# Kernel tuning notes

Hardware: AMD Instinct MI355X
Metric: run time of the kernel (lower is better)

The kernel has to match this reference:

```python
import jax, jax.numpy as jnp
import numpy as np

B, S, D = 64, 196, 768           # batch, num_tokens, dim
E, K = 4, 2                      # num experts (MoM internal default), top-k routing
TH = int(S * 1.0)                # token-mixing hidden (hidden_ratio=1.0)
MH = int(D * 4.0)                # channel MLP hidden (mlp_ratio=4.0)
EPS = 1e-6


def _ln(x, g, b):
    mu = jnp.mean(x, axis=-1, keepdims=True)
    var = jnp.mean((x - mu) ** 2, axis=-1, keepdims=True)
    return (x - mu) / jnp.sqrt(var + EPS) * g + b


def setup_inputs() -> dict:
    key = jax.random.key(0)
    ks = jax.random.split(key, 8)
    w = lambda k, sh: jax.random.normal(k, sh, dtype=jnp.float32) * 0.02
    return {
        "x": jax.random.normal(ks[0], (B, S, D), dtype=jnp.float32),
        "gamma1": jnp.ones((D,), jnp.float32), "beta1": jnp.zeros((D,), jnp.float32),
        "Wg": w(ks[1], (D, E)), "bg": jnp.zeros((E,), jnp.float32),
        "W1": w(ks[2], (E, S, TH)), "b1": jnp.zeros((E, TH), jnp.float32),
        "W2": w(ks[3], (E, TH, S)), "b2": jnp.zeros((E, S), jnp.float32),
        "gamma2": jnp.ones((D,), jnp.float32), "beta2": jnp.zeros((D,), jnp.float32),
        "Wm1": w(ks[4], (D, MH)), "bm1": jnp.zeros((MH,), jnp.float32),
        "Wm2": w(ks[5], (MH, D)), "bm2": jnp.zeros((D,), jnp.float32),
    }


def reference(x, gamma1, beta1, Wg, bg, W1, b1, W2, b2,
              gamma2, beta2, Wm1, bm1, Wm2, bm2):
    # --- pre-norm 1 + MoM token mixer ---
    normed = _ln(x, gamma1, beta1)                               # [B,S,D]
    logits = jnp.mean(normed, axis=1) @ Wg + bg                  # [B,E] per-sample router
    probs = jax.nn.softmax(logits, axis=-1)
    topv, topi = jax.lax.top_k(probs, K)                         # [B,K]
    topv = topv / jnp.sum(topv, axis=-1, keepdims=True)          # renormalize top-k
    combine = jnp.zeros((B, E), probs.dtype).at[jnp.arange(B)[:, None], topi].set(topv)
    xt = jnp.transpose(normed, (0, 2, 1))                        # [B,D,S] mix over tokens
    h = jax.nn.gelu(jnp.einsum('bds,esh->bedh', xt, W1) + b1[None, :, None, :],
                    approximate=False)                           # [B,E,D,TH]
    o = jnp.einsum('bedh,ehs->beds', h, W2) + b2[None, :, None, :]  # [B,E,D,S]
    mom_out = jnp.einsum('be,beds->bsd', combine, o)             # [B,S,D]
    x1 = x + mom_out
    # --- pre-norm 2 + channel MLP ---
    n2 = _ln(x1, gamma2, beta2)
    mlp = jax.nn.gelu(n2 @ Wm1 + bm1, approximate=False) @ Wm2 + bm2
    out = x1 + mlp
    # --- Switch-style load-balancing aux loss ---
    mask = (combine > 0).astype(probs.dtype)                     # [B,E]
    aux_loss = E * jnp.sum(jnp.mean(mask, axis=0) * jnp.mean(probs, axis=0))
    return out, aux_loss
```

## Files before the change

### kernel.cpp

```cpp
#include <hip/hip_runtime.h>
#include <hip/hip_bf16.h>
#include <math.h>

#define BB 64
#define SS 196
#define DD 768
#define EE 4
#define KKE 2
#define THH 196
#define MHH 3072
#define N1 (BB*SS*DD)
#define MM (BB*SS)
#define PP 256

typedef __bf16 bf16x8 __attribute__((ext_vector_type(8)));
typedef float f32x4 __attribute__((ext_vector_type(4)));

__device__ __forceinline__ float gelu_exact(float x){
    return 0.5f * x * (1.0f + erff(x * 0.70710678118654752f));
}

__global__ __launch_bounds__(256) void ln_bf16_kernel(const float* __restrict__ x,
                                                      const float* __restrict__ g,
                                                      const float* __restrict__ b,
                                                      __hip_bfloat16* __restrict__ out,
                                                      float* __restrict__ muo,
                                                      float* __restrict__ rso){
    int row = blockIdx.x;
    int tid = threadIdx.x;
    const float* xr = x + (size_t)row * DD;
    float v0 = xr[tid], v1 = xr[tid+256], v2 = xr[tid+512];
    float s = v0+v1+v2, ss = v0*v0+v1*v1+v2*v2;
    __shared__ float sh[10];
    int lane = tid & 63, wid = tid >> 6;
    #pragma unroll
    for (int o=32;o>0;o>>=1){ s += __shfl_down(s,o); ss += __shfl_down(ss,o); }
    if (lane==0){ sh[wid]=s; sh[4+wid]=ss; }
    __syncthreads();
    if (tid==0){
        float S1=sh[0]+sh[1]+sh[2]+sh[3], S2=sh[4]+sh[5]+sh[6]+sh[7];
        float mu = S1/DD; float var = S2/DD - mu*mu;
        float rs = rsqrtf(var + 1e-6f);
        sh[8]=mu; sh[9]=rs;
        muo[row]=mu; rso[row]=rs;
    }
    __syncthreads();
    float mu=sh[8], rs=sh[9];
    __hip_bfloat16* orow = out + (size_t)row*DD;
    orow[tid]     = __float2bfloat16((v0-mu)*rs*g[tid]     + b[tid]);
    orow[tid+256] = __float2bfloat16((v1-mu)*rs*g[tid+256] + b[tid+256]);
    orow[tid+512] = __float2bfloat16((v2-mu)*rs*g[tid+512] + b[tid+512]);
}

__global__ __launch_bounds__(256) void transpose_bf16_kernel(const float* __restrict__ src,
                                                             __hip_bfloat16* __restrict__ dst,
                                                             int R, int C){
    __shared__ float t[32][33];
    int c0 = blockIdx.x*32, r0 = blockIdx.y*32;
    int tx = threadIdx.x & 31, ty = threadIdx.x >> 5;
    #pragma unroll
    for (int rr = ty; rr < 32; rr += 8)
        t[rr][tx] = src[(size_t)(r0+rr)*C + c0 + tx];
    __syncthreads();
    #pragma unroll
    for (int cc = ty; cc < 32; cc += 8)
        dst[(size_t)(c0+cc)*R + r0 + tx] = __float2bfloat16(t[tx][cc]);
}

__global__ __launch_bounds__(256) void transpose_pad_w_kernel(const float* __restrict__ src0,
                                                              __hip_bfloat16* __restrict__ dst0,
                                                              int R, int C){
    const float* src = src0 + (size_t)blockIdx.z*R*C;
    __hip_bfloat16* dst = dst0 + (size_t)blockIdx.z*PP*PP;
    __shared__ float t[32][33];
    int c0 = blockIdx.x*32, r0 = blockIdx.y*32;
    int tx = threadIdx.x & 31, ty = threadIdx.x >> 5;
    #pragma unroll
    for (int rr = ty; rr < 32; rr += 8)
        t[rr][tx] = (r0+rr < R && c0+tx < C) ? src[(size_t)(r0+rr)*C + c0 + tx] : 0.f;
    __syncthreads();
    #pragma unroll
    for (int cc = ty; cc < 32; cc += 8)
        dst[(size_t)(c0+cc)*PP + r0 + tx] = __float2bfloat16(t[tx][cc]);
}

__global__ __launch_bounds__(256) void transpose_pad_n_kernel(const __hip_bfloat16* __restrict__ src,
                                                              __hip_bfloat16* __restrict__ dst){
    int b = blockIdx.z;
    __shared__ __hip_bfloat16 t[64][66];
    int d0 = blockIdx.x*64, s0 = blockIdx.y*64;
    int lane = threadIdx.x & 63, q = threadIdx.x >> 6;
    for (int i=q; i<64; i+=4){
        int s = s0+i;
        t[i][lane] = (s < SS) ? src[((size_t)b*SS + s)*DD + d0 + lane]
                              : __float2bfloat16(0.f);
    }
    __syncthreads();
    for (int i=q; i<64; i+=4){
        int d = d0+i;
        dst[((size_t)b*DD + d)*PP + s0 + lane] = t[lane][i];
    }
}

__global__ __launch_bounds__(384) void meanvec_kernel(const float* __restrict__ x,
                                                      const float* __restrict__ mu,
                                                      const float* __restrict__ rs,
                                                      const float* __restrict__ g1,
                                                      const float* __restrict__ b1,
                                                      float* __restrict__ mv){
    int b = blockIdx.y, d = blockIdx.x*384 + threadIdx.x;
    __shared__ float smu[SS], srs[SS];
    for (int s=threadIdx.x; s<SS; s+=384){ smu[s]=mu[b*SS+s]; srs[s]=rs[b*SS+s]; }
    __syncthreads();
    const float* base = x + (size_t)b*SS*DD + d;
    float a0=0.f, a1=0.f;
    for (int s=0;s<SS;s+=2){
        a0 += (base[(size_t)s*DD]     - smu[s])  * srs[s];
        a1 += (base[(size_t)(s+1)*DD] - smu[s+1])* srs[s+1];
    }
    mv[(size_t)b*DD + d] = g1[d]*((a0+a1)/(float)SS) + b1[d];
}

__global__ __launch_bounds__(64) void logits_kernel(const float* __restrict__ mv,
                                                    const float* __restrict__ Wg,
                                                    const float* __restrict__ bg,
                                                    float* __restrict__ combine,
                                                    float* __restrict__ probs,
                                                    int* __restrict__ topi,
                                                    float* __restrict__ topw){
    int b = blockIdx.x, lane = threadIdx.x;
    float pl[EE] = {0.f,0.f,0.f,0.f};
    #pragma unroll
    for (int i=0;i<DD/64;++i){
        int d = lane + i*64;
        float m = mv[(size_t)b*DD + d];
        #pragma unroll
        for (int e=0;e<EE;++e) pl[e] += m * Wg[d*EE + e];
    }
    #pragma unroll
    for (int e=0;e<EE;++e){
        #pragma unroll
        for (int o=32;o>0;o>>=1) pl[e] += __shfl_down(pl[e], o);
    }
    if (lane==0){
        float lg[EE];
        for (int e=0;e<EE;++e) lg[e] = pl[e] + bg[e];
        float mx = lg[0];
        for (int e=1;e<EE;++e) mx = fmaxf(mx, lg[e]);
        float p[EE]; float sum=0.f;
        for (int e=0;e<EE;++e){ p[e]=expf(lg[e]-mx); sum+=p[e]; }
        for (int e=0;e<EE;++e) p[e] /= sum;
        int i0=0; for (int e=1;e<EE;++e) if (p[e]>p[i0]) i0=e;
        int i1=-1;
        for (int e=0;e<EE;++e){ if (e==i0) continue; if (i1<0 || p[e]>p[i1]) i1=e; }
        float v0=p[i0], v1=p[i1], rsum=v0+v1;
        float w0=v0/rsum, w1=v1/rsum;
        for (int e=0;e<EE;++e){ probs[b*EE+e]=p[e]; combine[b*EE+e]=0.f; }
        combine[b*EE+i0]=w0; combine[b*EE+i1]=w1;
        topi[b*KKE]=i0; topi[b*KKE+1]=i1;
        topw[b*KKE]=w0; topw[b*KKE+1]=w1;
    }
}

__global__ __launch_bounds__(256) void aux_kernel(const float* __restrict__ combine,
                                                  const float* __restrict__ probs,
                                                  float* __restrict__ aux_out){
    int tid = threadIdx.x; int e = tid>>6, b = tid&63;
    float m = combine[b*EE+e] > 0.f ? 1.f : 0.f;
    float p = probs[b*EE+e];
    #pragma unroll
    for (int o=32;o>0;o>>=1){ m += __shfl_down(m,o); p += __shfl_down(p,o); }
    __shared__ float sh[EE];
    if ((tid&63)==0) sh[e] = (m/(float)BB)*(p/(float)BB);
    __syncthreads();
    if (tid==0) aux_out[0] = (float)EE * (sh[0]+sh[1]+sh[2]+sh[3]);
}

__global__ __launch_bounds__(256) void tok_gemm1_kernel(
    const __hip_bfloat16* __restrict__ nTp,
    const __hip_bfloat16* __restrict__ w1tp,
    const float* __restrict__ b1,
    const int* __restrict__ topi,
    __hip_bfloat16* __restrict__ htok)
{
    __shared__ __hip_bfloat16 As[128*64];
    __shared__ __hip_bfloat16 Bs[128*64];
    int tid=threadIdx.x, lane=tid&63, w=tid>>6;
    int wm=w>>1, wn=w&1, l15=lane&15, l4=lane>>4;
    int be = blockIdx.z, b = be>>1;
    int e = __builtin_amdgcn_readfirstlane(topi[b*KKE + (be&1)]);
    int m0 = blockIdx.y*128, n0 = blockIdx.x*128;
    const __hip_bfloat16* A  = nTp  + ((size_t)b*DD + m0)*PP;
    const __hip_bfloat16* Bt = w1tp + ((size_t)e*PP + n0)*PP;
    f32x4 acc[4][4];
    #pragma unroll
    for (int mi=0;mi<4;++mi)
        #pragma unroll
        for (int ni=0;ni<4;++ni) acc[mi][ni] = (f32x4){0.f,0.f,0.f,0.f};

    int srow = w*32 + (lane>>3), sc = lane&7;
    int soff = srow*64 + ((sc ^ (srow&7))<<3);
    const __hip_bfloat16* Ap = A + (size_t)srow*PP + sc*8;
    const __hip_bfloat16* Bp = Bt + (size_t)srow*PP + sc*8;
    bf16x8 va[4], vb[4];
    #pragma unroll
    for (int i=0;i<4;++i){
        va[i] = *reinterpret_cast<const bf16x8*>(Ap + (size_t)i*8*PP);
        vb[i] = *reinterpret_cast<const bf16x8*>(Bp + (size_t)i*8*PP);
    }
    for (int k0=0; k0<PP; k0+=64){
        __syncthreads();
        #pragma unroll
        for (int i=0;i<4;++i){
            *reinterpret_cast<bf16x8*>(&As[soff + i*8*64]) = va[i];
            *reinterpret_cast<bf16x8*>(&Bs[soff + i*8*64]) = vb[i];
        }
        __syncthreads();
        if (k0+64 < PP){
            #pragma unroll
            for (int i=0;i<4;++i){
                va[i] = *reinterpret_cast<const bf16x8*>(Ap + (size_t)i*8*PP + (k0+64));
                vb[i] = *reinterpret_cast<const bf16x8*>(Bp + (size_t)i*8*PP + (k0+64));
            }
        }
        #pragma unroll
        for (int kk=0;kk<2;++kk){
            bf16x8 af[4], bfr[4];
            #pragma unroll
            for (int mi=0;mi<4;++mi){
                int r = wm*64 + mi*16 + l15, kc = kk*4 + l4;
                af[mi] = *reinterpret_cast<const bf16x8*>(&As[r*64 + ((kc ^ (r&7))<<3)]);
            }
            #pragma unroll
            for (int ni=0;ni<4;++ni){
                int r = wn*64 + ni*16 + l15, kc = kk*4 + l4;
                bfr[ni] = *reinterpret_cast<const bf16x8*>(&Bs[r*64 + ((kc ^ (r&7))<<3)]);
            }
            #pragma unroll
            for (int mi=0;mi<4;++mi)
                #pragma unroll
                for (int ni=0;ni<4;++ni)
                    acc[mi][ni] = __builtin_amdgcn_mfma_f32_16x16x32_bf16(af[mi], bfr[ni], acc[mi][ni], 0, 0, 0);
        }
    }
    #pragma unroll
    for (int mi=0;mi<4;++mi){
        #pragma unroll
        for (int ni=0;ni<4;++ni){
            int col = n0 + wn*64 + ni*16 + l15;
            float bv = (col < THH) ? b1[e*THH + col] : 0.f;
            #pragma unroll
            for (int r=0;r<4;++r){
                int row = m0 + wm*64 + mi*16 + l4*4 + r;
                float v = (col < THH) ? gelu_exact(acc[mi][ni][r] + bv) : 0.f;
                htok[((size_t)be*DD + row)*PP + col] = __float2bfloat16(v);
            }
        }
    }
}

__global__ __launch_bounds__(256) void tok_gemm2_kernel(
    const __hip_bfloat16* __restrict__ htok,
    const __hip_bfloat16* __restrict__ w2tp,
    const float* __restrict__ b2,
    const int* __restrict__ topi, const float* __restrict__ topw,
    const float* __restrict__ x, float* __restrict__ x1)
{
    __shared__ __hip_bfloat16 As[128*64];
    __shared__ __hip_bfloat16 Bs[128*64];
    int tid=threadIdx.x, lane=tid&63, w=tid>>6;
    int wm=w>>1, wn=w&1, l15=lane&15, l4=lane>>4;
    int b = blockIdx.z;
    int m0 = blockIdx.y*128, n0 = blockIdx.x*128;
    float w0 = topw[b*KKE], w1 = topw[b*KKE+1];
    f32x4 acc[4][4];
    #pragma unroll
    for (int mi=0;mi<4;++mi)
        #pragma unroll
        for (int ni=0;ni<4;++ni) acc[mi][ni] = (f32x4){0.f,0.f,0.f,0.f};

    int srow = w*32 + (lane>>3), sc = lane&7;
    int soff = srow*64 + ((sc ^ (srow&7))<<3);

    for (int pass=0; pass<2; ++pass){
        int e = __builtin_amdgcn_readfirstlane(topi[b*KKE + pass]);
        const __hip_bfloat16* Ap = htok + ((size_t)(b*KKE+pass)*DD + m0 + srow)*PP + sc*8;
        const __hip_bfloat16* Bp = w2tp + ((size_t)e*PP + n0 + srow)*PP + sc*8;
        bf16x8 va[4], vb[4];
        #pragma unroll
        for (int i=0;i<4;++i){
            va[i] = *reinterpret_cast<const bf16x8*>(Ap + (size_t)i*8*PP);
            vb[i] = *reinterpret_cast<const bf16x8*>(Bp + (size_t)i*8*PP);
        }
        for (int k0=0; k0<PP; k0+=64){
            __syncthreads();
            #pragma unroll
            for (int i=0;i<4;++i){
                *reinterpret_cast<bf16x8*>(&As[soff + i*8*64]) = va[i];
                *reinterpret_cast<bf16x8*>(&Bs[soff + i*8*64]) = vb[i];
            }
            __syncthreads();
            if (k0+64 < PP){
                #pragma unroll
                for (int i=0;i<4;++i){
                    va[i] = *reinterpret_cast<const bf16x8*>(Ap + (size_t)i*8*PP + (k0+64));
                    vb[i] = *reinterpret_cast<const bf16x8*>(Bp + (size_t)i*8*PP + (k0+64));
                }
            }
            #pragma unroll
            for (int kk=0;kk<2;++kk){
                bf16x8 af[4], bfr[4];
                #pragma unroll
                for (int mi=0;mi<4;++mi){
                    int r = wm*64 + mi*16 + l15, kc = kk*4 + l4;
                    af[mi] = *reinterpret_cast<const bf16x8*>(&As[r*64 + ((kc ^ (r&7))<<3)]);
                }
                #pragma unroll
                for (int ni=0;ni<4;++ni){
                    int r = wn*64 + ni*16 + l15, kc = kk*4 + l4;
                    bfr[ni] = *reinterpret_cast<const bf16x8*>(&Bs[r*64 + ((kc ^ (r&7))<<3)]);
                }
                #pragma unroll
                for (int mi=0;mi<4;++mi)
                    #pragma unroll
                    for (int ni=0;ni<4;++ni)
                        acc[mi][ni] = __builtin_amdgcn_mfma_f32_16x16x32_bf16(af[mi], bfr[ni], acc[mi][ni], 0, 0, 0);
            }
        }
        if (pass==0){
            float sc0 = w0 / w1;
            #pragma unroll
            for (int mi=0;mi<4;++mi)
                #pragma unroll
                for (int ni=0;ni<4;++ni)
                    #pragma unroll
                    for (int r=0;r<4;++r) acc[mi][ni][r] *= sc0;
        }
    }
    int e0 = topi[b*KKE], e1 = topi[b*KKE+1];
    #pragma unroll
    for (int mi=0;mi<4;++mi){
        #pragma unroll
        for (int ni=0;ni<4;++ni){
            int col = n0 + wn*64 + ni*16 + l15;
            if (col < SS){
                float bias = w0*b2[e0*SS+col] + w1*b2[e1*SS+col];
                int rowb = m0 + wm*64 + mi*16 + l4*4;
                size_t idx = ((size_t)b*SS + col)*DD + rowb;
                f32x4 xv = *reinterpret_cast<const f32x4*>(x + idx);
                f32x4 res;
                #pragma unroll
                for (int r=0;r<4;++r) res[r] = xv[r] + w1*acc[mi][ni][r] + bias;
                *reinterpret_cast<f32x4*>(x1 + idx) = res;
            }
        }
    }
}

__global__ __launch_bounds__(256) void tokenmix2_kernel(
    const __hip_bfloat16* __restrict__ nbf, const float* __restrict__ x,
    const float* __restrict__ W1, const float* __restrict__ b1,
    const float* __restrict__ W2, const float* __restrict__ b2,
    const int* __restrict__ topi, const float* __restrict__ topw,
    float* __restrict__ x1)
{
    __shared__ __hip_bfloat16 xs[SS][64];
    __shared__ __hip_bfloat16 Hs[THH][64];
    int b = blockIdx.y, d0 = blockIdx.x*64;
    int tid = threadIdx.x, lane = tid&63, w = tid>>6;
    for (int s = w; s < SS; s += 4)
        xs[s][lane] = nbf[((size_t)b*SS + s)*DD + d0 + lane];
    #pragma unroll
    for (int k=0;k<KKE;++k){
        int e = __builtin_amdgcn_readfirstlane(topi[b*KKE+k]);
        float wgt = topw[b*KKE+k];
        __syncthreads();
        const float* W1e = W1 + (size_t)e*SS*THH;
        for (int hj=0; hj<13; ++hj){
            int hb = w + 16*hj;
            if (hj < 12){
                float a0=b1[e*THH+hb], a1=b1[e*THH+hb+4], a2=b1[e*THH+hb+8], a3=b1[e*THH+hb+12];
                for (int s=0;s<SS;++s){
                    float xv = __bfloat162float(xs[s][lane]);
                    const float* wr = W1e + (size_t)s*THH + hb;
                    a0 += xv*wr[0]; a1 += xv*wr[4]; a2 += xv*wr[8]; a3 += xv*wr[12];
                }
                Hs[hb][lane]    = __float2bfloat16(gelu_exact(a0));
                Hs[hb+4][lane]  = __float2bfloat16(gelu_exact(a1));
                Hs[hb+8][lane]  = __float2bfloat16(gelu_exact(a2));
                Hs[hb+12][lane] = __float2bfloat16(gelu_exact(a3));
            } else {
                float a0=b1[e*THH+hb];
                for (int s=0;s<SS;++s)
                    a0 += __bfloat162float(xs[s][lane]) * W1e[(size_t)s*THH + hb];
                Hs[hb][lane] = __float2bfloat16(gelu_exact(a0));
            }
        }
        __syncthreads();
        const float* W2e = W2 + (size_t)e*THH*SS;
        for (int sj=0; sj<13; ++sj){
            int sb = w + 16*sj;
            if (sj < 12){
                float o0=b2[e*SS+sb], o1=b2[e*SS+sb+4], o2=b2[e*SS+sb+8], o3=b2[e*SS+sb+12];
                for (int h=0;h<THH;++h){
                    float hv = __bfloat162float(Hs[h][lane]);
                    const float* wr = W2e + (size_t)h*SS + sb;
                    o0 += hv*wr[0]; o1 += hv*wr[4]; o2 += hv*wr[8]; o3 += hv*wr[12];
                }
                float ov[4] = {o0,o1,o2,o3};
                #pragma unroll
                for (int u=0;u<4;++u){
                    size_t idx = ((size_t)b*SS + sb + 4*u)*DD + d0 + lane;
                    float val = wgt*ov[u];
                    if (k==0) x1[idx] = x[idx] + val; else x1[idx] += val;
                }
            } else {
                float o0=b2[e*SS+sb];
                for (int h=0;h<THH;++h)
                    o0 += __bfloat162float(Hs[h][lane]) * W2e[(size_t)h*SS + sb];
                size_t idx = ((size_t)b*SS + sb)*DD + d0 + lane;
                float val = wgt*o0;
                if (k==0) x1[idx] = x[idx] + val; else x1[idx] += val;
            }
        }
    }
}

template<int KDIM, int EPI>
__global__ __launch_bounds__(256) void gemm_bt_kernel(
    const __hip_bfloat16* __restrict__ A,
    const __hip_bfloat16* __restrict__ Bt,
    const float* __restrict__ bias,
    __hip_bfloat16* __restrict__ Hout,
    float* __restrict__ Cio,
    int Ntot)
{
    __shared__ __hip_bfloat16 As[128*64];
    __shared__ __hip_bfloat16 Bs[128*64];
    int tid = threadIdx.x, lane = tid&63, w = tid>>6;
    int wm = w>>1, wn = w&1;
    int l15 = lane&15, l4 = lane>>4;
    int m0 = blockIdx.y*128, n0 = blockIdx.x*128;
    f32x4 acc[4][4];
    #pragma unroll
    for (int mi=0;mi<4;++mi)
        #pragma unroll
        for (int ni=0;ni<4;++ni) acc[mi][ni] = (f32x4){0.f,0.f,0.f,0.f};

    int srow = w*32 + (lane>>3);
    int sc   = lane&7;
    int soff = srow*64 + ((sc ^ (srow&7))<<3);
    const __hip_bfloat16* Ap = A  + (size_t)(m0+srow)*KDIM + sc*8;
    const __hip_bfloat16* Bp = Bt + (size_t)(n0+srow)*KDIM + sc*8;

    bf16x8 va[4], vb[4];
    #pragma unroll
    for (int i=0;i<4;++i){
        va[i] = *reinterpret_cast<const bf16x8*>(Ap + (size_t)i*8*KDIM);
        vb[i] = *reinterpret_cast<const bf16x8*>(Bp + (size_t)i*8*KDIM);
    }
    for (int k0=0; k0<KDIM; k0+=64){
        __syncthreads();
        #pragma unroll
        for (int i=0;i<4;++i){
            *reinterpret_cast<bf16x8*>(&As[soff + i*8*64]) = va[i];
            *reinterpret_cast<bf16x8*>(&Bs[soff + i*8*64]) = vb[i];
        }
        __syncthreads();
        if (k0+64 < KDIM){
            #pragma unroll
            for (int i=0;i<4;++i){
                va[i] = *reinterpret_cast<const bf16x8*>(Ap + (size_t)i*8*KDIM + (k0+64));
                vb[i] = *reinterpret_cast<const bf16x8*>(Bp + (size_t)i*8*KDIM + (k0+64));
            }
        }
        #pragma unroll
        for (int kk=0;kk<2;++kk){
            bf16x8 af[4], bfr[4];
            #pragma unroll
            for (int mi=0;mi<4;++mi){
                int r = wm*64 + mi*16 + l15;
                int kc = kk*4 + l4;
                af[mi] = *reinterpret_cast<const bf16x8*>(&As[r*64 + ((kc ^ (r&7))<<3)]);
            }
            #pragma unroll
            for (int ni=0;ni<4;++ni){
                int r = wn*64 + ni*16 + l15;
                int kc = kk*4 + l4;
                bfr[ni] = *reinterpret_cast<const bf16x8*>(&Bs[r*64 + ((kc ^ (r&7))<<3)]);
            }
            #pragma unroll
            for (int mi=0;mi<4;++mi)
                #pragma unroll
                for (int ni=0;ni<4;++ni)
                    acc[mi][ni] = __builtin_amdgcn_mfma_f32_16x16x32_bf16(af[mi], bfr[ni], acc[mi][ni], 0, 0, 0);
        }
    }
    #pragma unroll
    for (int mi=0;mi<4;++mi){
        #pragma unroll
        for (int ni=0;ni<4;++ni){
            int col = n0 + wn*64 + ni*16 + l15;
            float bv = bias[col];
            #pragma unroll
            for (int r=0;r<4;++r){
                int row = m0 + wm*64 + mi*16 + l4*4 + r;
                if (EPI==0)
                    Hout[(size_t)row*Ntot + col] = __float2bfloat16(gelu_exact(acc[mi][ni][r] + bv));
                else
                    Cio[(size_t)row*Ntot + col] += acc[mi][ni][r] + bv;
            }
        }
    }
}

__global__ __launch_bounds__(512, 4) void mlp_mfma_kernel(
    const __hip_bfloat16* __restrict__ n2b,
    const __hip_bfloat16* __restrict__ w1t,
    const float* __restrict__ bm1,
    const __hip_bfloat16* __restrict__ w2t,
    const float* __restrict__ bm2,
    float* __restrict__ io)
{
    __shared__ __align__(16) __hip_bfloat16 Ht[32*64];
    int tid = threadIdx.x;
    int wid = tid >> 6, lane = tid & 63;
    int wm = wid >> 2, wn = wid & 3;
    int l15 = lane & 15, l4 = lane >> 4;
    int m0 = blockIdx.x * 32;
    f32x4 acc[12];
    #pragma unroll
    for (int f=0; f<12; ++f) acc[f] = (f32x4){0.f,0.f,0.f,0.f};
    const __hip_bfloat16* aptr = n2b + (size_t)(m0 + wm*16 + l15)*DD + l4*8;
    for (int hc = 0; hc < MHH; hc += 64) {
        f32x4 h = (f32x4){0.f,0.f,0.f,0.f};
        const __hip_bfloat16* bptr = w1t + (size_t)(hc + wn*16 + l15)*DD + l4*8;
        #pragma unroll 4
        for (int ks = 0; ks < DD; ks += 32) {
            bf16x8 a = *reinterpret_cast<const bf16x8*>(aptr + ks);
            bf16x8 bb = *reinterpret_cast<const bf16x8*>(bptr + ks);
            h = __builtin_amdgcn_mfma_f32_16x16x32_bf16(a, bb, h, 0, 0, 0);
        }
        float bv = bm1[hc + wn*16 + l15];
        __syncthreads();
        {
            int col = wn*16 + l15;
            int chunk = col >> 3, inner = col & 7;
            #pragma unroll
            for (int r=0; r<4; ++r) {
                int row = wm*16 + l4*4 + r;
                float v = gelu_exact(h[r] + bv);
                Ht[row*64 + ((chunk ^ (row&7))<<3) + inner] = __float2bfloat16(v);
            }
        }
        __syncthreads();
        #pragma unroll
        for (int kk = 0; kk < 2; ++kk) {
            int arow = wm*16 + l15;
            int ach = (kk*32 + l4*8) >> 3;
            bf16x8 aH = *reinterpret_cast<const bf16x8*>(&Ht[arow*64 + ((ach ^ (arow&7))<<3)]);
            const __hip_bfloat16* b2p = w2t + (size_t)(wn*192 + l15)*MHH + hc + kk*32 + l4*8;
            #pragma unroll
            for (int f=0; f<12; ++f) {
                bf16x8 bb = *reinterpret_cast<const bf16x8*>(b2p + (size_t)f*16*MHH);
                acc[f] = __builtin_amdgcn_mfma_f32_16x16x32_bf16(aH, bb, acc[f], 0, 0, 0);
            }
        }
    }
    #pragma unroll
    for (int f=0; f<12; ++f) {
        int col = wn*192 + f*16 + l15;
        float b2v = bm2[col];
        #pragma unroll
        for (int r=0; r<4; ++r) {
            size_t idx = (size_t)(m0 + wm*16 + l4*4 + r)*DD + col;
            io[idx] += acc[f][r] + b2v;
        }
    }
}

extern "C" void kernel_launch(void* const* d_in, const int* in_sizes, int n_in,
                              void* d_out, int out_size, void* d_ws, size_t ws_size,
                              hipStream_t stream) {
    const float* x    = (const float*)d_in[0];
    const float* g1   = (const float*)d_in[1];
    const float* be1  = (const float*)d_in[2];
    const float* Wg   = (const float*)d_in[3];
    const float* bg   = (const float*)d_in[4];
    const float* W1   = (const float*)d_in[5];
    const float* b1e  = (const float*)d_in[6];
    const float* W2   = (const float*)d_in[7];
    const float* b2e  = (const float*)d_in[8];
    const float* g2   = (const float*)d_in[9];
    const float* be2  = (const float*)d_in[10];
    const float* Wm1  = (const float*)d_in[11];
    const float* bm1  = (const float*)d_in[12];
    const float* Wm2  = (const float*)d_in[13];
    const float* bm2  = (const float*)d_in[14];

    float* out = (float*)d_out;
    char* w = (char*)d_ws;

    const size_t OFF_W1T  = 19267584;
    const size_t OFF_W2T  = OFF_W1T + 4718592;
    const size_t OFF_W1TP = OFF_W2T + 4718592;
    const size_t OFF_W2TP = OFF_W1TP + (size_t)EE*PP*PP*2;
    const size_t OFF_REG  = OFF_W2TP + (size_t)EE*PP*PP*2;
    const size_t NTP_B    = (size_t)BB*DD*PP*2;
    const size_t HTOK_B   = (size_t)BB*KKE*DD*PP*2;
    const size_t HMLP_B   = (size_t)MM*MHH*2;
    const size_t REG_B    = (NTP_B + HTOK_B > HMLP_B) ? (NTP_B + HTOK_B) : HMLP_B;
    const size_t REG_END  = OFF_REG + REG_B;
    const size_t NEED     = REG_END + 400000;
    bool bigws = (ws_size >= NEED);

    __hip_bfloat16* nbf  = (__hip_bfloat16*)w;
    __hip_bfloat16* w1t  = (__hip_bfloat16*)(w + OFF_W1T);
    __hip_bfloat16* w2t  = (__hip_bfloat16*)(w + OFF_W2T);
    __hip_bfloat16* w1tp = (__hip_bfloat16*)(w + OFF_W1TP);
    __hip_bfloat16* w2tp = (__hip_bfloat16*)(w + OFF_W2TP);
    __hip_bfloat16* nTp  = (__hip_bfloat16*)(w + OFF_REG);
    __hip_bfloat16* htok = (__hip_bfloat16*)(w + OFF_REG + NTP_B);
    __hip_bfloat16* Hmlp = (__hip_bfloat16*)(w + OFF_REG);

    size_t tail = bigws ? REG_END : OFF_W1TP;
    float* muv     = (float*)(w + tail);
    float* rsigv   = muv + MM;
    float* mv      = rsigv + MM;
    float* combine = mv + (size_t)BB*DD;
    float* probs   = combine + BB*EE;
    float* topw    = probs + BB*EE;
    int*   topi    = (int*)(topw + BB*KKE);

    transpose_bf16_kernel<<<dim3(MHH/32, DD/32), 256, 0, stream>>>(Wm1, w1t, DD, MHH);
    transpose_bf16_kernel<<<dim3(DD/32, MHH/32), 256, 0, stream>>>(Wm2, w2t, MHH, DD);
    if (bigws){
        transpose_pad_w_kernel<<<dim3(PP/32, PP/32, EE), 256, 0, stream>>>(W1, w1tp, SS, THH);
        transpose_pad_w_kernel<<<dim3(PP/32, PP/32, EE), 256, 0, stream>>>(W2, w2tp, THH, SS);
    }
    ln_bf16_kernel<<<MM, 256, 0, stream>>>(x, g1, be1, nbf, muv, rsigv);
    meanvec_kernel<<<dim3(2, BB), 384, 0, stream>>>(x, muv, rsigv, g1, be1, mv);
    logits_kernel<<<BB, 64, 0, stream>>>(mv, Wg, bg, combine, probs, topi, topw);
    aux_kernel<<<1, 256, 0, stream>>>(combine, probs, out + N1);
    if (bigws){
        transpose_pad_n_kernel<<<dim3(DD/64, PP/64, BB), 256, 0, stream>>>(nbf, nTp);
        tok_gemm1_kernel<<<dim3(PP/128, DD/128, BB*KKE), 256, 0, stream>>>(nTp, w1tp, b1e, topi, htok);
        tok_gemm2_kernel<<<dim3(PP/128, DD/128, BB), 256, 0, stream>>>(htok, w2tp, b2e, topi, topw, x, out);
    } else {
        tokenmix2_kernel<<<dim3(DD/64, BB), 256, 0, stream>>>(nbf, x, W1, b1e, W2, b2e,
                                                              topi, topw, out);
    }
    ln_bf16_kernel<<<MM, 256, 0, stream>>>(out, g2, be2, nbf, muv, rsigv);
    if (bigws){
        gemm_bt_kernel<DD, 0><<<dim3(MHH/128, MM/128), 256, 0, stream>>>(
            nbf, w1t, bm1, Hmlp, nullptr, MHH);
        gemm_bt_kernel<MHH, 1><<<dim3(DD/128, MM/128), 256, 0, stream>>>(
            Hmlp, w2t, bm2, nullptr, out, DD);
    } else {
        mlp_mfma_kernel<<<MM/32, 512, 0, stream>>>(nbf, w1t, bm1, w2t, bm2, out);
    }
}
```

Baseline: 383.5 us.

## Stage GEMM tiles with direct global-to-LDS loads instead of register prefetch

Replaces the register-staged prefetch (global load to VGPRs, then ds_write) in the three GEMM kernels with global_load_lds 16-byte direct transfers into shared memory. This cuts VGPR pressure and the LDS write instructions. In exchange it drops the XOR swizzle, since direct LDS loads write linearly, which may bring back LDS bank conflicts on fragment reads. It also removes the overlap of next-tile global loads with MFMA compute, because loads are now issued and waited on inside each k-step.

```diff
diff --git a/kernel.cpp b/kernel.cpp
--- a/kernel.cpp
+++ b/kernel.cpp
@@ -18,6 +18,23 @@
 
 __device__ __forceinline__ float gelu_exact(float x){
     return 0.5f * x * (1.0f + erff(x * 0.70710678118654752f));
+}
+
+#define GLD16(ldsp, gp) \
+    __builtin_amdgcn_global_load_lds((__attribute__((address_space(1))) void*)(gp), \
+                                     (__attribute__((address_space(3))) void*)(ldsp), 16, 0, 0)
+
+__device__ __forceinline__ void stage_tiles(__hip_bfloat16* As, __hip_bfloat16* Bs,
+                                            const __hip_bfloat16* Ag, const __hip_bfloat16* Bg,
+                                            size_t kstride, int k0, int w, int lane){
+    #pragma unroll
+    for (int i=0;i<4;++i){
+        int cb = i*256 + w*64;
+        int cg = cb + lane;
+        int row = cg>>3, col = (cg&7)*8;
+        GLD16(As + (size_t)cb*8, Ag + (size_t)row*kstride + k0 + col);
+        GLD16(Bs + (size_t)cb*8, Bg + (size_t)row*kstride + k0 + col);
+    }
 }
 
 __global__ __launch_bounds__(256) void ln_bf16_kernel(const float* __restrict__ x,
@@ -190,51 +207,30 @@
     int be = blockIdx.z, b = be>>1;
     int e = __builtin_amdgcn_readfirstlane(topi[b*KKE + (be&1)]);
     int m0 = blockIdx.y*128, n0 = blockIdx.x*128;
-    const __hip_bfloat16* A  = nTp  + ((size_t)b*DD + m0)*PP;
-    const __hip_bfloat16* Bt = w1tp + ((size_t)e*PP + n0)*PP;
+    const __hip_bfloat16* Ag = nTp  + ((size_t)b*DD + m0)*PP;
+    const __hip_bfloat16* Bg = w1tp + ((size_t)e*PP + n0)*PP;
     f32x4 acc[4][4];
     #pragma unroll
     for (int mi=0;mi<4;++mi)
         #pragma unroll
         for (int ni=0;ni<4;++ni) acc[mi][ni] = (f32x4){0.f,0.f,0.f,0.f};
 
-    int srow = w*32 + (lane>>3), sc = lane&7;
-    int soff = srow*64 + ((sc ^ (srow&7))<<3);
-    const __hip_bfloat16* Ap = A + (size_t)srow*PP + sc*8;
-    const __hip_bfloat16* Bp = Bt + (size_t)srow*PP + sc*8;
-    bf16x8 va[4], vb[4];
-    #pragma unroll
-    for (int i=0;i<4;++i){
-        va[i] = *reinterpret_cast<const bf16x8*>(Ap + (size_t)i*8*PP);
-        vb[i] = *reinterpret_cast<const bf16x8*>(Bp + (size_t)i*8*PP);
-    }
     for (int k0=0; k0<PP; k0+=64){
         __syncthreads();
-        #pragma unroll
-        for (int i=0;i<4;++i){
-            *reinterpret_cast<bf16x8*>(&As[soff + i*8*64]) = va[i];
-            *reinterpret_cast<bf16x8*>(&Bs[soff + i*8*64]) = vb[i];
-        }
-        __syncthreads();
-        if (k0+64 < PP){
-            #pragma unroll
-            for (int i=0;i<4;++i){
-                va[i] = *reinterpret_cast<const bf16x8*>(Ap + (size_t)i*8*PP + (k0+64));
-                vb[i] = *reinterpret_cast<const bf16x8*>(Bp + (size_t)i*8*PP + (k0+64));
-            }
-        }
+        stage_tiles(As, Bs, Ag, Bg, PP, k0, w, lane);
+        __syncthreads();
         #pragma unroll
         for (int kk=0;kk<2;++kk){
             bf16x8 af[4], bfr[4];
             #pragma unroll
             for (int mi=0;mi<4;++mi){
                 int r = wm*64 + mi*16 + l15, kc = kk*4 + l4;
-                af[mi] = *reinterpret_cast<const bf16x8*>(&As[r*64 + ((kc ^ (r&7))<<3)]);
+                af[mi] = *reinterpret_cast<const bf16x8*>(&As[r*64 + kc*8]);
             }
             #pragma unroll
             for (int ni=0;ni<4;++ni){
                 int r = wn*64 + ni*16 + l15, kc = kk*4 + l4;
-                bfr[ni] = *reinterpret_cast<const bf16x8*>(&Bs[r*64 + ((kc ^ (r&7))<<3)]);
+                bfr[ni] = *reinterpret_cast<const bf16x8*>(&Bs[r*64 + kc*8]);
             }
             #pragma unroll
             for (int mi=0;mi<4;++mi)
@@ -279,46 +275,26 @@
         #pragma unroll
         for (int ni=0;ni<4;++ni) acc[mi][ni] = (f32x4){0.f,0.f,0.f,0.f};
 
-    int srow = w*32 + (lane>>3), sc = lane&7;
-    int soff = srow*64 + ((sc ^ (srow&7))<<3);
-
     for (int pass=0; pass<2; ++pass){
         int e = __builtin_amdgcn_readfirstlane(topi[b*KKE + pass]);
-        const __hip_bfloat16* Ap = htok + ((size_t)(b*KKE+pass)*DD + m0 + srow)*PP + sc*8;
-        const __hip_bfloat16* Bp = w2tp + ((size_t)e*PP + n0 + srow)*PP + sc*8;
-        bf16x8 va[4], vb[4];
-        #pragma unroll
-        for (int i=0;i<4;++i){
-            va[i] = *reinterpret_cast<const bf16x8*>(Ap + (size_t)i*8*PP);
-            vb[i] = *reinterpret_cast<const bf16x8*>(Bp + (size_t)i*8*PP);
-        }
+        const __hip_bfloat16* Ag = htok + ((size_t)(b*KKE+pass)*DD + m0)*PP;
+        const __hip_bfloat16* Bg = w2tp + ((size_t)e*PP + n0)*PP;
         for (int k0=0; k0<PP; k0+=64){
             __syncthreads();
-            #pragma unroll
-            for (int i=0;i<4;++i){
-                *reinterpret_cast<bf16x8*>(&As[soff + i*8*64]) = va[i];
-                *reinterpret_cast<bf16x8*>(&Bs[soff + i*8*64]) = vb[i];
-            }
+            stage_tiles(As, Bs, Ag, Bg, PP, k0, w, lane);
             __syncthreads();
-            if (k0+64 < PP){
-                #pragma unroll
-                for (int i=0;i<4;++i){
-                    va[i] = *reinterpret_cast<const bf16x8*>(Ap + (size_t)i*8*PP + (k0+64));
-                    vb[i] = *reinterpret_cast<const bf16x8*>(Bp + (size_t)i*8*PP + (k0+64));
-                }
-            }
             #pragma unroll
             for (int kk=0;kk<2;++kk){
                 bf16x8 af[4], bfr[4];
                 #pragma unroll
                 for (int mi=0;mi<4;++mi){
                     int r = wm*64 + mi*16 + l15, kc = kk*4 + l4;
-                    af[mi] = *reinterpret_cast<const bf16x8*>(&As[r*64 + ((kc ^ (r&7))<<3)]);
+                    af[mi] = *reinterpret_cast<const bf16x8*>(&As[r*64 + kc*8]);
                 }
                 #pragma unroll
                 for (int ni=0;ni<4;++ni){
                     int r = wn*64 + ni*16 + l15, kc = kk*4 + l4;
-                    bfr[ni] = *reinterpret_cast<const bf16x8*>(&Bs[r*64 + ((kc ^ (r&7))<<3)]);
+                    bfr[ni] = *reinterpret_cast<const bf16x8*>(&Bs[r*64 + kc*8]);
                 }
                 #pragma unroll
                 for (int mi=0;mi<4;++mi)
@@ -441,39 +417,18 @@
     int wm = w>>1, wn = w&1;
     int l15 = lane&15, l4 = lane>>4;
     int m0 = blockIdx.y*128, n0 = blockIdx.x*128;
+    const __hip_bfloat16* Ag = A  + (size_t)m0*KDIM;
+    const __hip_bfloat16* Bg = Bt + (size_t)n0*KDIM;
     f32x4 acc[4][4];
     #pragma unroll
     for (int mi=0;mi<4;++mi)
         #pragma unroll
         for (int ni=0;ni<4;++ni) acc[mi][ni] = (f32x4){0.f,0.f,0.f,0.f};
 
-    int srow = w*32 + (lane>>3);
-    int sc   = lane&7;
-    int soff = srow*64 + ((sc ^ (srow&7))<<3);
-    const __hip_bfloat16* Ap = A  + (size_t)(m0+srow)*KDIM + sc*8;
-    const __hip_bfloat16* Bp = Bt + (size_t)(n0+srow)*KDIM + sc*8;
-
-    bf16x8 va[4], vb[4];
-    #pragma unroll
-    for (int i=0;i<4;++i){
-        va[i] = *reinterpret_cast<const bf16x8*>(Ap + (size_t)i*8*KDIM);
-        vb[i] = *reinterpret_cast<const bf16x8*>(Bp + (size_t)i*8*KDIM);
-    }
     for (int k0=0; k0<KDIM; k0+=64){
         __syncthreads();
-        #pragma unroll
-        for (int i=0;i<4;++i){
-            *reinterpret_cast<bf16x8*>(&As[soff + i*8*64]) = va[i];
-            *reinterpret_cast<bf16x8*>(&Bs[soff + i*8*64]) = vb[i];
-        }
-        __syncthreads();
-        if (k0+64 < KDIM){
-            #pragma unroll
-            for (int i=0;i<4;++i){
-                va[i] = *reinterpret_cast<const bf16x8*>(Ap + (size_t)i*8*KDIM + (k0+64));
-                vb[i] = *reinterpret_cast<const bf16x8*>(Bp + (size_t)i*8*KDIM + (k0+64));
-            }
-        }
+        stage_tiles(As, Bs, Ag, Bg, KDIM, k0, w, lane);
+        __syncthreads();
         #pragma unroll
         for (int kk=0;kk<2;++kk){
             bf16x8 af[4], bfr[4];
@@ -481,13 +436,13 @@
             for (int mi=0;mi<4;++mi){
                 int r = wm*64 + mi*16 + l15;
                 int kc = kk*4 + l4;
-                af[mi] = *reinterpret_cast<const bf16x8*>(&As[r*64 + ((kc ^ (r&7))<<3)]);
+                af[mi] = *reinterpret_cast<const bf16x8*>(&As[r*64 + kc*8]);
             }
             #pragma unroll
             for (int ni=0;ni<4;++ni){
                 int r = wn*64 + ni*16 + l15;
                 int kc = kk*4 + l4;
-                bfr[ni] = *reinterpret_cast<const bf16x8*>(&Bs[r*64 + ((kc ^ (r&7))<<3)]);
+                bfr[ni] = *reinterpret_cast<const bf16x8*>(&Bs[r*64 + kc*8]);
             }
             #pragma unroll
             for (int mi=0;mi<4;++mi)
```

Result: slower. 441.2 us (+15.0%).
